# Kernel tuning notes

Hardware: AMD Instinct MI355X
Metric: run time of the kernel (lower is better)

Reference implementation:

```python
import jax, jax.numpy as jnp
import numpy as np
from jax import lax

B, C_IN, L = 512, 32, 512
E = 8
POOL = 16            # AdaptiveAvgPool1d(16)
D_IN = C_IN * L      # expert input = flattened x
D_OUT = 768          # pooler_output dim (hard-coded in module)
TAU = 1.0            # gumbel temperature
BN_EPS = 1e-5


def setup_inputs() -> dict:
    key = jax.random.key(0)
    ks = jax.random.split(key, 8)
    s = 0.02
    return {
        "x": jax.random.normal(ks[0], (B, C_IN, L), jnp.float32),
        "gumbel_u": jax.random.uniform(ks[1], (B, E), jnp.float32, 1e-6, 1.0 - 1e-6),
        "conv_w": jax.random.normal(ks[2], (64, C_IN, 3), jnp.float32) * s,
        "conv_b": jnp.zeros((64,), jnp.float32),
        "bn_gamma": jnp.ones((64 * POOL,), jnp.float32),
        "bn_beta": jnp.zeros((64 * POOL,), jnp.float32),
        "bn_mean": jnp.zeros((64 * POOL,), jnp.float32),
        "bn_var": jnp.ones((64 * POOL,), jnp.float32),
        "fc1_w": jax.random.normal(ks[3], (128, 64 * POOL), jnp.float32) * s,
        "fc1_b": jnp.zeros((128,), jnp.float32),
        "fc2_w": jax.random.normal(ks[4], (E, 128), jnp.float32) * s,
        "fc2_b": jnp.zeros((E,), jnp.float32),
        "expert_w": jax.random.normal(ks[5], (E, D_IN, D_OUT), jnp.float32) * s,
        "expert_b": jnp.zeros((E, D_OUT), jnp.float32),
    }


def _gelu(v):
    return jax.nn.gelu(v, approximate=False)  # torch nn.GELU default (erf)


def reference(x, gumbel_u, conv_w, conv_b, bn_gamma, bn_beta, bn_mean, bn_var,
              fc1_w, fc1_b, fc2_w, fc2_b, expert_w, expert_b):
    # ---- router ----
    h = lax.conv_general_dilated(x, conv_w, (1,), ((1, 1),),
                                 dimension_numbers=("NCH", "OIH", "NCH"))
    h = _gelu(h + conv_b[None, :, None])                     # [B,64,L]
    h = h.reshape(B, 64, POOL, L // POOL).mean(-1)           # adaptive avg pool -> [B,64,16]
    h = h.reshape(B, 64 * POOL)                              # flatten
    h = (h - bn_mean) * lax.rsqrt(bn_var + BN_EPS) * bn_gamma + bn_beta  # BN (eval)
    h = _gelu(h @ fc1_w.T + fc1_b)                           # dropout inactive in eval
    logits = h @ fc2_w.T + fc2_b                             # [B,E]

    # ---- soft gumbel-softmax gating (hard=False), then top-2 ----
    g = -jnp.log(-jnp.log(gumbel_u))
    routing_weights = jax.nn.softmax((logits + g) / TAU, axis=1)
    topv, topi = lax.top_k(routing_weights, 2)               # [B,2]
    w = topv / (topv.sum(axis=1, keepdims=True) + 1e-8)      # [B,2]

    # ---- dispatch/compute/combine (dense-expert stand-in: flatten + linear) ----
    xf = x.reshape(B, D_IN)
    all_out = jnp.einsum("bd,edh->beh", xf, expert_w) + expert_b[None]  # [B,E,768]
    sel = jnp.take_along_axis(all_out, topi[:, :, None], axis=1)        # [B,2,768]
    pooler_output = (sel * w[:, :, None]).sum(axis=1)                   # [B,768]
    return pooler_output
```

## Files before the change

### kernel.cpp

```cpp
#include <hip/hip_runtime.h>
#include <hip/hip_bf16.h>

#define NB 512
#define CIN 32
#define LEN 512
#define NE 8
#define NPOOL 16
#define DIN 16384
#define DOUT 768
#define HD 1024
#define F1 128

#define MT 256
#define NT 128
#define BK 64

typedef __attribute__((ext_vector_type(4))) float f32x4;
typedef __attribute__((ext_vector_type(8))) short s16x8;
typedef __attribute__((ext_vector_type(4))) unsigned int u32x4;

__device__ __forceinline__ float gelu_erf(float v) {
    return 0.5f * v * (1.0f + erff(v * 0.70710678118654752f));
}

__device__ __forceinline__ unsigned cvt_pk(float lo, float hi) {
    unsigned r;
    asm volatile("v_cvt_pk_bf16_f32 %0, %1, %2" : "=v"(r) : "v"(lo), "v"(hi));
    return r;
}

__global__ __launch_bounds__(512) void krouter_conv(
    const float* __restrict__ x, const float* __restrict__ cw, const float* __restrict__ cb,
    const float* __restrict__ bng, const float* __restrict__ bnb,
    const float* __restrict__ bnm, const float* __restrict__ bnv,
    float* __restrict__ h)
{
    __shared__ float xs[CIN * LEN];
    int b = blockIdx.x;
    int t = threadIdx.x;

    const f32x4* xg = (const f32x4*)(x + (size_t)b * DIN);
    #pragma unroll
    for (int u = 0; u < 8; ++u) {
        int fi = t + 512 * u;
        f32x4 v = xg[fi];
        int e0 = fi * 4;
        int ci = e0 >> 9, l = e0 & 511;
        int byte = ci * 2048 + ((l * 4) ^ ((((unsigned)l >> 5) & 7u) << 4));
        *(f32x4*)((char*)xs + byte) = v;
    }
    __syncthreads();

    int p  = t & 15;
    int cq = t >> 4;
    int co0 = cq * 2, co1 = co0 + 1;
    int l0 = p * 32;

    float sa[32], sb[32];
    #pragma unroll
    for (int i = 0; i < 32; ++i) { sa[i] = 0.f; sb[i] = 0.f; }

    for (int ci = 0; ci < CIN; ++ci) {
        float f[40];
        #pragma unroll
        for (int u = 0; u < 10; ++u) {
            int l = l0 - 4 + 4 * u;
            int lc = min(max(l, 0), 508);
            int byte = ci * 2048 + ((lc * 4) ^ ((((unsigned)lc >> 5) & 7u) << 4));
            f32x4 v = *(const f32x4*)((const char*)xs + byte);
            f[4*u+0] = v[0]; f[4*u+1] = v[1]; f[4*u+2] = v[2]; f[4*u+3] = v[3];
        }
        if (p == 0)  f[3]  = 0.f;
        if (p == 15) f[36] = 0.f;
        float wa0 = cw[co0*96 + ci*3 + 0], wa1 = cw[co0*96 + ci*3 + 1], wa2 = cw[co0*96 + ci*3 + 2];
        float wb0 = cw[co1*96 + ci*3 + 0], wb1 = cw[co1*96 + ci*3 + 1], wb2 = cw[co1*96 + ci*3 + 2];
        #pragma unroll
        for (int i = 0; i < 32; ++i) {
            sa[i] = fmaf(f[i+3], wa0, fmaf(f[i+4], wa1, fmaf(f[i+5], wa2, sa[i])));
            sb[i] = fmaf(f[i+3], wb0, fmaf(f[i+4], wb1, fmaf(f[i+5], wb2, sb[i])));
        }
    }

    float ba = cb[co0], bbv = cb[co1];
    float ma = 0.f, mb = 0.f;
    #pragma unroll
    for (int i = 0; i < 32; ++i) { ma += gelu_erf(sa[i] + ba); mb += gelu_erf(sb[i] + bbv); }
    ma *= (1.f / 32.f); mb *= (1.f / 32.f);

    int oa = co0 * NPOOL + p, ob = co1 * NPOOL + p;
    float ra = (ma - bnm[oa]) * rsqrtf(bnv[oa] + 1e-5f) * bng[oa] + bnb[oa];
    float rb = (mb - bnm[ob]) * rsqrtf(bnv[ob] + 1e-5f) * bng[ob] + bnb[ob];
    h[(size_t)b * HD + oa] = ra;
    h[(size_t)b * HD + ob] = rb;
}

__global__ __launch_bounds__(256) void krouter_fc(
    const float* __restrict__ h, const float* __restrict__ f1w, const float* __restrict__ f1b,
    const float* __restrict__ f2w, const float* __restrict__ f2b,
    const float* __restrict__ gu,
    int* __restrict__ top2e, float* __restrict__ top2w,
    int* __restrict__ cnt, int* __restrict__ rowlist, float* __restrict__ roww)
{
    __shared__ float hs[8 * HD];
    __shared__ float h1s[8 * F1];
    __shared__ float lg[8 * NE];

    int bb = blockIdx.x * 8;
    int t = threadIdx.x;

    const f32x4* hg = (const f32x4*)(h + (size_t)bb * HD);
    f32x4* hs4 = (f32x4*)hs;
    #pragma unroll
    for (int u = 0; u < 8; ++u) hs4[t + 256 * u] = hg[t + 256 * u];
    __syncthreads();

    int j = t & 127;
    int pr = t >> 7;
    float acc[4] = {0.f, 0.f, 0.f, 0.f};
    const f32x4* w4 = (const f32x4*)(f1w + (size_t)j * HD);
    for (int k4 = 0; k4 < 256; ++k4) {
        f32x4 w = w4[k4];
        #pragma unroll
        for (int g = 0; g < 4; ++g) {
            f32x4 hv = hs4[(pr * 4 + g) * 256 + k4];
            acc[g] += w[0]*hv[0] + w[1]*hv[1] + w[2]*hv[2] + w[3]*hv[3];
        }
    }
    float bj = f1b[j];
    #pragma unroll
    for (int g = 0; g < 4; ++g) h1s[(pr * 4 + g) * F1 + j] = gelu_erf(acc[g] + bj);
    __syncthreads();

    if (t < 64) {
        int bi = t >> 3, e = t & 7;
        float s = f2b[e];
        const float* w = f2w + e * F1;
        const float* hh = h1s + bi * F1;
        #pragma unroll 8
        for (int k = 0; k < F1; ++k) s += hh[k] * w[k];
        lg[bi * NE + e] = s;
    }
    __syncthreads();

    if (t < 8) {
        int bi = t; int b = bb + bi;
        float r[NE];
        float mx = -1e30f;
        #pragma unroll
        for (int e = 0; e < NE; ++e) {
            float g = -logf(-logf(gu[b * NE + e]));
            r[e] = lg[bi * NE + e] + g;
            mx = fmaxf(mx, r[e]);
        }
        float sum = 0.f;
        #pragma unroll
        for (int e = 0; e < NE; ++e) { r[e] = expf(r[e] - mx); sum += r[e]; }
        float inv = 1.f / sum;
        #pragma unroll
        for (int e = 0; e < NE; ++e) r[e] *= inv;
        int e0 = 0; float v0 = r[0];
        #pragma unroll
        for (int e = 1; e < NE; ++e) if (r[e] > v0) { v0 = r[e]; e0 = e; }
        int e1 = -1; float v1 = -1.f;
        #pragma unroll
        for (int e = 0; e < NE; ++e) { if (e == e0) continue; if (r[e] > v1) { v1 = r[e]; e1 = e; } }
        float den = v0 + v1 + 1e-8f;
        float w0 = v0 / den, w1 = v1 / den;
        top2e[b * 2 + 0] = e0; top2e[b * 2 + 1] = e1;
        top2w[b * 2 + 0] = w0; top2w[b * 2 + 1] = w1;
        int p0 = atomicAdd(&cnt[e0], 1);
        rowlist[e0 * NB + p0] = b * 2 + 0; roww[e0 * NB + p0] = w0;
        int p1 = atomicAdd(&cnt[e1], 1);
        rowlist[e1 * NB + p1] = b * 2 + 1; roww[e1 * NB + p1] = w1;
    }
}

__global__ __launch_bounds__(512) void kgemm(
    const float* __restrict__ x, const float* __restrict__ ew,
    const int* __restrict__ cnt, const int* __restrict__ rowlist, const float* __restrict__ roww,
    float* __restrict__ ypart, int nkc, int kch)
{
    int bid = blockIdx.x;
    int kc = bid % nkc;
    int nt = (bid / nkc) % 6;
    int e  = bid / (nkc * 6);
    int cn = cnt[e];
    if (cn <= 0) return;

    __shared__ __align__(16) short As[MT * BK];
    __shared__ __align__(16) short Bs[NT * BK];

    int t = threadIdx.x;
    int wid = t >> 6, lane = t & 63;
    int wm = wid >> 1, wn = wid & 1;
    int g = lane >> 4;
    int NS = kch / BK;
    int k0 = kc * kch;

    int bn = t & 127, bkg = t >> 7;
    const float* bwp = ew + (size_t)e * ((size_t)DIN * DOUT)
                          + (size_t)(k0 + bkg * 16) * DOUT + nt * NT + bn;

    for (int row0 = 0; row0 < cn; row0 += MT) {
        int mloc = min(MT, cn - row0);

        int ar = t >> 1, ah = t & 1;
        int arc = min(ar, mloc - 1);
        int ent_a = rowlist[e * NB + row0 + arc];
        const float* axp = x + (size_t)(ent_a >> 1) * DIN + k0 + ah * 32;
        bool ado = (ar < mloc);
        bool wact = (wm * 64 < mloc);

        f32x4 acc[4][4];
        #pragma unroll
        for (int i = 0; i < 4; ++i)
            #pragma unroll
            for (int jj = 0; jj < 4; ++jj) acc[i][jj] = (f32x4){0.f, 0.f, 0.f, 0.f};

        f32x4 Ar[8]; float Br[16];
        if (ado) {
            const f32x4* p = (const f32x4*)axp;
            #pragma unroll
            for (int u = 0; u < 8; ++u) Ar[u] = p[u];
        }
        #pragma unroll
        for (int u = 0; u < 2; ++u)
            #pragma unroll
            for (int i = 0; i < 8; ++i)
                Br[u*8+i] = bwp[(size_t)(u*8+i) * DOUT];

        for (int s = 0; s < NS; ++s) {
            if (ado) {
                #pragma unroll
                for (int u = 0; u < 4; ++u) {
                    u32x4 pk;
                    pk[0] = cvt_pk(Ar[2*u][0], Ar[2*u][1]);
                    pk[1] = cvt_pk(Ar[2*u][2], Ar[2*u][3]);
                    pk[2] = cvt_pk(Ar[2*u+1][0], Ar[2*u+1][1]);
                    pk[3] = cvt_pk(Ar[2*u+1][2], Ar[2*u+1][3]);
                    int col = ah * 32 + u * 8;
                    *(u32x4*)((char*)As + ar * 128 + ((col * 2) ^ ((ar & 7) << 4))) = pk;
                }
            }
            {
                #pragma unroll
                for (int u = 0; u < 2; ++u) {
                    u32x4 pk;
                    pk[0] = cvt_pk(Br[u*8+0], Br[u*8+1]);
                    pk[1] = cvt_pk(Br[u*8+2], Br[u*8+3]);
                    pk[2] = cvt_pk(Br[u*8+4], Br[u*8+5]);
                    pk[3] = cvt_pk(Br[u*8+6], Br[u*8+7]);
                    int col = bkg * 16 + u * 8;
                    *(u32x4*)((char*)Bs + bn * 128 + ((col * 2) ^ ((bn & 7) << 4))) = pk;
                }
            }
            __syncthreads();

            if (s + 1 < NS) {
                if (ado) {
                    const f32x4* p = (const f32x4*)(axp + (s + 1) * BK);
                    #pragma unroll
                    for (int u = 0; u < 8; ++u) Ar[u] = p[u];
                }
                #pragma unroll
                for (int u = 0; u < 2; ++u)
                    #pragma unroll
                    for (int i = 0; i < 8; ++i)
                        Br[u*8+i] = bwp[(size_t)((s + 1) * BK + u*8 + i) * DOUT];
            }

            if (wact) {
                #pragma unroll
                for (int kk = 0; kk < 2; ++kk) {
                    int colb = (kk * 32 + g * 8) * 2;
                    s16x8 af[4], bfr[4];
                    #pragma unroll
                    for (int mi = 0; mi < 4; ++mi) {
                        int m = wm * 64 + mi * 16 + (lane & 15);
                        af[mi] = *(const s16x8*)((const char*)As + m * 128 + (colb ^ ((m & 7) << 4)));
                    }
                    #pragma unroll
                    for (int ni = 0; ni < 4; ++ni) {
                        int n = wn * 64 + ni * 16 + (lane & 15);
                        bfr[ni] = *(const s16x8*)((const char*)Bs + n * 128 + (colb ^ ((n & 7) << 4)));
                    }
                    #pragma unroll
                    for (int mi = 0; mi < 4; ++mi)
                        #pragma unroll
                        for (int ni = 0; ni < 4; ++ni)
                            acc[mi][ni] = __builtin_amdgcn_mfma_f32_16x16x32_bf16(af[mi], bfr[ni], acc[mi][ni], 0, 0, 0);
                }
            }
            __syncthreads();
        }

        if (wact) {
            #pragma unroll
            for (int mi = 0; mi < 4; ++mi) {
                #pragma unroll
                for (int rg = 0; rg < 4; ++rg) {
                    int m = wm * 64 + mi * 16 + g * 4 + rg;
                    if (m < mloc) {
                        int ent = rowlist[e * NB + row0 + m];
                        float wgt = roww[e * NB + row0 + m];
                        int ob = ent >> 1, slot = ent & 1;
                        float* dst = ypart + ((size_t)(slot * nkc + kc) * NB + ob) * DOUT
                                   + nt * NT + wn * 64 + (lane & 15);
                        #pragma unroll
                        for (int ni = 0; ni < 4; ++ni)
                            dst[ni * 16] = acc[mi][ni][rg] * wgt;
                    }
                }
            }
        }
    }
}

__global__ __launch_bounds__(256) void kcombine(
    const float* __restrict__ ypart,
    const int* __restrict__ top2e, const float* __restrict__ top2w,
    const float* __restrict__ eb, float* __restrict__ out, int nplanes)
{
    int b = blockIdx.y;
    int n = blockIdx.x * 256 + threadIdx.x;
    float s = 0.f;
    for (int p = 0; p < nplanes; ++p) s += ypart[((size_t)p * NB + b) * DOUT + n];
    int e0 = top2e[b * 2], e1 = top2e[b * 2 + 1];
    float w0 = top2w[b * 2], w1 = top2w[b * 2 + 1];
    s += w0 * eb[e0 * DOUT + n] + w1 * eb[e1 * DOUT + n];
    out[(size_t)b * DOUT + n] = s;
}

extern "C" void kernel_launch(void* const* d_in, const int* in_sizes, int n_in,
                              void* d_out, int out_size, void* d_ws, size_t ws_size,
                              hipStream_t stream)
{
    const float* x   = (const float*)d_in[0];
    const float* gu  = (const float*)d_in[1];
    const float* cw  = (const float*)d_in[2];
    const float* cb  = (const float*)d_in[3];
    const float* bng = (const float*)d_in[4];
    const float* bnb = (const float*)d_in[5];
    const float* bnm = (const float*)d_in[6];
    const float* bnv = (const float*)d_in[7];
    const float* f1w = (const float*)d_in[8];
    const float* f1b = (const float*)d_in[9];
    const float* f2w = (const float*)d_in[10];
    const float* f2b = (const float*)d_in[11];
    const float* ew  = (const float*)d_in[12];
    const float* eb  = (const float*)d_in[13];

    int nkc = (ws_size >= (size_t)56 * 1024 * 1024) ? 16 : 8;
    int kch = DIN / nkc;

    char* ws = (char*)d_ws;
    size_t off = 0;
    float* h       = (float*)(ws + off); off += (size_t)NB * HD * 4;
    int*   top2e   = (int*)(ws + off);   off += (size_t)NB * 2 * 4;
    float* top2w   = (float*)(ws + off); off += (size_t)NB * 2 * 4;
    int*   cnt     = (int*)(ws + off);   off += 256;
    int*   rowlist = (int*)(ws + off);   off += (size_t)NE * NB * 4;
    float* roww    = (float*)(ws + off); off += (size_t)NE * NB * 4;
    float* ypart   = (float*)(ws + off); off += (size_t)2 * nkc * NB * DOUT * 4;

    hipMemsetAsync(cnt, 0, NE * sizeof(int), stream);
    krouter_conv<<<NB, 512, 0, stream>>>(x, cw, cb, bng, bnb, bnm, bnv, h);
    krouter_fc<<<NB / 8, 256, 0, stream>>>(h, f1w, f1b, f2w, f2b, gu,
                                           top2e, top2w, cnt, rowlist, roww);
    kgemm<<<NE * 6 * nkc, 512, 0, stream>>>(x, ew, cnt, rowlist, roww, ypart, nkc, kch);
    kcombine<<<dim3(3, NB), 256, 0, stream>>>(ypart, top2e, top2w, eb, (float*)d_out, 2 * nkc);
}
```

Before: 254.2 us.

## Shrink expert GEMM tiles, reorder LDS staging, store bf16 partials, drop memset

Halves the expert GEMM tile to 128x64 with 256-thread blocks and launch bounds that allow four blocks per CU, doubling the grid so more of the GPU stays busy. The K loop is reordered so the next tile's global loads are issued before the MFMAs and converted into LDS after a barrier. Split-K partial results are now written as bf16 instead of fp32, which halves partial-buffer traffic and lowers the workspace needed for the 16-way split. The counter memset is folded into the router conv kernel. The bf16 partials add rounding error across the 32 summed planes, and the smaller tiles reuse each loaded tile less.

```diff
diff --git a/kernel.cpp b/kernel.cpp
--- a/kernel.cpp
+++ b/kernel.cpp
@@ -11,8 +11,8 @@
 #define HD 1024
 #define F1 128
 
-#define MT 256
-#define NT 128
+#define MT 128
+#define NT 64
 #define BK 64
 
 typedef __attribute__((ext_vector_type(4))) float f32x4;
@@ -29,15 +29,22 @@
     return r;
 }
 
+__device__ __forceinline__ unsigned short f2bf_u(float f) {
+    union { float f; unsigned u; } x; x.f = f;
+    unsigned r = x.u + 0x7fffu + ((x.u >> 16) & 1u);
+    return (unsigned short)(r >> 16);
+}
+
 __global__ __launch_bounds__(512) void krouter_conv(
     const float* __restrict__ x, const float* __restrict__ cw, const float* __restrict__ cb,
     const float* __restrict__ bng, const float* __restrict__ bnb,
     const float* __restrict__ bnm, const float* __restrict__ bnv,
-    float* __restrict__ h)
+    float* __restrict__ h, int* __restrict__ cnt)
 {
     __shared__ float xs[CIN * LEN];
     int b = blockIdx.x;
     int t = threadIdx.x;
+    if (b == 0 && t < NE) cnt[t] = 0;
 
     const f32x4* xg = (const f32x4*)(x + (size_t)b * DIN);
     #pragma unroll
@@ -175,15 +182,15 @@
     }
 }
 
-__global__ __launch_bounds__(512) void kgemm(
+__global__ __launch_bounds__(256, 4) void kgemm(
     const float* __restrict__ x, const float* __restrict__ ew,
     const int* __restrict__ cnt, const int* __restrict__ rowlist, const float* __restrict__ roww,
-    float* __restrict__ ypart, int nkc, int kch)
+    unsigned short* __restrict__ ypart, int nkc, int kch)
 {
     int bid = blockIdx.x;
     int kc = bid % nkc;
-    int nt = (bid / nkc) % 6;
-    int e  = bid / (nkc * 6);
+    int nt = (bid / nkc) % 12;
+    int e  = bid / (nkc * 12);
     int cn = cnt[e];
     if (cn <= 0) return;
 
@@ -197,7 +204,7 @@
     int NS = kch / BK;
     int k0 = kc * kch;
 
-    int bn = t & 127, bkg = t >> 7;
+    int bn = t & 63, bkg = t >> 6;
     const float* bwp = ew + (size_t)e * ((size_t)DIN * DOUT)
                           + (size_t)(k0 + bkg * 16) * DOUT + nt * NT + bn;
 
@@ -211,25 +218,25 @@
         bool ado = (ar < mloc);
         bool wact = (wm * 64 < mloc);
 
-        f32x4 acc[4][4];
+        f32x4 acc[4][2];
         #pragma unroll
         for (int i = 0; i < 4; ++i)
             #pragma unroll
-            for (int jj = 0; jj < 4; ++jj) acc[i][jj] = (f32x4){0.f, 0.f, 0.f, 0.f};
+            for (int jj = 0; jj < 2; ++jj) acc[i][jj] = (f32x4){0.f, 0.f, 0.f, 0.f};
 
         f32x4 Ar[8]; float Br[16];
-        if (ado) {
-            const f32x4* p = (const f32x4*)axp;
+
+        auto issue_loads = [&](int s) {
+            const f32x4* p = (const f32x4*)(axp + s * BK);
+            if (ado) {
+                #pragma unroll
+                for (int u = 0; u < 8; ++u) Ar[u] = p[u];
+            }
             #pragma unroll
-            for (int u = 0; u < 8; ++u) Ar[u] = p[u];
-        }
-        #pragma unroll
-        for (int u = 0; u < 2; ++u)
-            #pragma unroll
-            for (int i = 0; i < 8; ++i)
-                Br[u*8+i] = bwp[(size_t)(u*8+i) * DOUT];
-
-        for (int s = 0; s < NS; ++s) {
+            for (int i = 0; i < 16; ++i)
+                Br[i] = bwp[(size_t)(s * BK + i) * DOUT];
+        };
+        auto cvt_store = [&]() {
             if (ado) {
                 #pragma unroll
                 for (int u = 0; u < 4; ++u) {
@@ -238,59 +245,53 @@
                     pk[1] = cvt_pk(Ar[2*u][2], Ar[2*u][3]);
                     pk[2] = cvt_pk(Ar[2*u+1][0], Ar[2*u+1][1]);
                     pk[3] = cvt_pk(Ar[2*u+1][2], Ar[2*u+1][3]);
-                    int col = ah * 32 + u * 8;
-                    *(u32x4*)((char*)As + ar * 128 + ((col * 2) ^ ((ar & 7) << 4))) = pk;
+                    int colb = (ah * 32 + u * 8) * 2;
+                    *(u32x4*)((char*)As + ar * 128 + (colb ^ ((ar & 7) << 4))) = pk;
                 }
             }
-            {
-                #pragma unroll
-                for (int u = 0; u < 2; ++u) {
-                    u32x4 pk;
-                    pk[0] = cvt_pk(Br[u*8+0], Br[u*8+1]);
-                    pk[1] = cvt_pk(Br[u*8+2], Br[u*8+3]);
-                    pk[2] = cvt_pk(Br[u*8+4], Br[u*8+5]);
-                    pk[3] = cvt_pk(Br[u*8+6], Br[u*8+7]);
-                    int col = bkg * 16 + u * 8;
-                    *(u32x4*)((char*)Bs + bn * 128 + ((col * 2) ^ ((bn & 7) << 4))) = pk;
-                }
-            }
-            __syncthreads();
-
-            if (s + 1 < NS) {
-                if (ado) {
-                    const f32x4* p = (const f32x4*)(axp + (s + 1) * BK);
-                    #pragma unroll
-                    for (int u = 0; u < 8; ++u) Ar[u] = p[u];
-                }
-                #pragma unroll
-                for (int u = 0; u < 2; ++u)
-                    #pragma unroll
-                    for (int i = 0; i < 8; ++i)
-                        Br[u*8+i] = bwp[(size_t)((s + 1) * BK + u*8 + i) * DOUT];
-            }
+            #pragma unroll
+            for (int u = 0; u < 2; ++u) {
+                u32x4 pk;
+                pk[0] = cvt_pk(Br[u*8+0], Br[u*8+1]);
+                pk[1] = cvt_pk(Br[u*8+2], Br[u*8+3]);
+                pk[2] = cvt_pk(Br[u*8+4], Br[u*8+5]);
+                pk[3] = cvt_pk(Br[u*8+6], Br[u*8+7]);
+                int colb = (bkg * 16 + u * 8) * 2;
+                *(u32x4*)((char*)Bs + bn * 128 + (colb ^ ((bn & 7) << 4))) = pk;
+            }
+        };
+
+        issue_loads(0);
+        cvt_store();
+        __syncthreads();
+
+        for (int s = 0; s < NS; ++s) {
+            if (s + 1 < NS) issue_loads(s + 1);
 
             if (wact) {
                 #pragma unroll
                 for (int kk = 0; kk < 2; ++kk) {
-                    int colb = (kk * 32 + g * 8) * 2;
-                    s16x8 af[4], bfr[4];
+                    int colb = kk * 64 + g * 16;
+                    s16x8 af[4], bfr[2];
                     #pragma unroll
                     for (int mi = 0; mi < 4; ++mi) {
                         int m = wm * 64 + mi * 16 + (lane & 15);
                         af[mi] = *(const s16x8*)((const char*)As + m * 128 + (colb ^ ((m & 7) << 4)));
                     }
                     #pragma unroll
-                    for (int ni = 0; ni < 4; ++ni) {
-                        int n = wn * 64 + ni * 16 + (lane & 15);
+                    for (int ni = 0; ni < 2; ++ni) {
+                        int n = wn * 32 + ni * 16 + (lane & 15);
                         bfr[ni] = *(const s16x8*)((const char*)Bs + n * 128 + (colb ^ ((n & 7) << 4)));
                     }
                     #pragma unroll
                     for (int mi = 0; mi < 4; ++mi)
                         #pragma unroll
-                        for (int ni = 0; ni < 4; ++ni)
+                        for (int ni = 0; ni < 2; ++ni)
                             acc[mi][ni] = __builtin_amdgcn_mfma_f32_16x16x32_bf16(af[mi], bfr[ni], acc[mi][ni], 0, 0, 0);
                 }
             }
+            __syncthreads();
+            if (s + 1 < NS) cvt_store();
             __syncthreads();
         }
 
@@ -304,11 +305,11 @@
                         int ent = rowlist[e * NB + row0 + m];
                         float wgt = roww[e * NB + row0 + m];
                         int ob = ent >> 1, slot = ent & 1;
-                        float* dst = ypart + ((size_t)(slot * nkc + kc) * NB + ob) * DOUT
-                                   + nt * NT + wn * 64 + (lane & 15);
+                        unsigned short* dst = ypart + ((size_t)(slot * nkc + kc) * NB + ob) * DOUT
+                                            + nt * NT + wn * 32 + (lane & 15);
                         #pragma unroll
-                        for (int ni = 0; ni < 4; ++ni)
-                            dst[ni * 16] = acc[mi][ni][rg] * wgt;
+                        for (int ni = 0; ni < 2; ++ni)
+                            dst[ni * 16] = f2bf_u(acc[mi][ni][rg] * wgt);
                     }
                 }
             }
@@ -317,14 +318,18 @@
 }
 
 __global__ __launch_bounds__(256) void kcombine(
-    const float* __restrict__ ypart,
+    const unsigned short* __restrict__ ypart,
     const int* __restrict__ top2e, const float* __restrict__ top2w,
     const float* __restrict__ eb, float* __restrict__ out, int nplanes)
 {
     int b = blockIdx.y;
     int n = blockIdx.x * 256 + threadIdx.x;
     float s = 0.f;
-    for (int p = 0; p < nplanes; ++p) s += ypart[((size_t)p * NB + b) * DOUT + n];
+    for (int p = 0; p < nplanes; ++p) {
+        unsigned v = ypart[((size_t)p * NB + b) * DOUT + n];
+        union { unsigned u; float f; } c; c.u = v << 16;
+        s += c.f;
+    }
     int e0 = top2e[b * 2], e1 = top2e[b * 2 + 1];
     float w0 = top2w[b * 2], w1 = top2w[b * 2 + 1];
     s += w0 * eb[e0 * DOUT + n] + w1 * eb[e1 * DOUT + n];
@@ -350,7 +355,7 @@
     const float* ew  = (const float*)d_in[12];
     const float* eb  = (const float*)d_in[13];
 
-    int nkc = (ws_size >= (size_t)56 * 1024 * 1024) ? 16 : 8;
+    int nkc = (ws_size >= (size_t)40 * 1024 * 1024) ? 16 : 8;
     int kch = DIN / nkc;
 
     char* ws = (char*)d_ws;
@@ -361,12 +366,12 @@
     int*   cnt     = (int*)(ws + off);   off += 256;
     int*   rowlist = (int*)(ws + off);   off += (size_t)NE * NB * 4;
     float* roww    = (float*)(ws + off); off += (size_t)NE * NB * 4;
-    float* ypart   = (float*)(ws + off); off += (size_t)2 * nkc * NB * DOUT * 4;
-
-    hipMemsetAsync(cnt, 0, NE * sizeof(int), stream);
-    krouter_conv<<<NB, 512, 0, stream>>>(x, cw, cb, bng, bnb, bnm, bnv, h);
+    unsigned short* ypart = (unsigned short*)(ws + off);
+    off += (size_t)2 * nkc * NB * DOUT * 2;
+
+    krouter_conv<<<NB, 512, 0, stream>>>(x, cw, cb, bng, bnb, bnm, bnv, h, cnt);
     krouter_fc<<<NB / 8, 256, 0, stream>>>(h, f1w, f1b, f2w, f2b, gu,
                                            top2e, top2w, cnt, rowlist, roww);
-    kgemm<<<NE * 6 * nkc, 512, 0, stream>>>(x, ew, cnt, rowlist, roww, ypart, nkc, kch);
+    kgemm<<<NE * 12 * nkc, 256, 0, stream>>>(x, ew, cnt, rowlist, roww, ypart, nkc, kch);
     kcombine<<<dim3(3, NB), 256, 0, stream>>>(ypart, top2e, top2w, eb, (float*)d_out, 2 * nkc);
 }
```

New measurement: 357.5 us. +40.6%, slower.
